# Optimization experiments

Hardware: AMD Instinct MI355X
Metric: run time of the kernel (lower is better)

## Reference

```python
import jax, jax.numpy as jnp
import numpy as np

B, N, C, HEADS, R = 8, 4096, 256, 8, 4  # N = H*W, R = reduction_ratio
LN_EPS = 1e-5


def setup_inputs() -> dict:
    key = jax.random.key(0)
    ks = jax.random.split(key, 6)
    sc = 0.02
    return {
        "x": jax.random.normal(ks[0], (B, N, C), jnp.float32),
        "conv_w": jax.random.normal(ks[1], (C, C, R, R), jnp.float32) * sc,  # OIHW
        "conv_b": jnp.zeros((C,), jnp.float32),
        "ln_g": jnp.ones((C,), jnp.float32),
        "ln_b": jnp.zeros((C,), jnp.float32),
        "kv_w": jax.random.normal(ks[2], (2 * C, C), jnp.float32) * sc,  # torch Linear (out,in)
        "kv_b": jnp.zeros((2 * C,), jnp.float32),
        "q_w": jax.random.normal(ks[3], (C, C), jnp.float32) * sc,
        "q_b": jnp.zeros((C,), jnp.float32),
        "out_w": jax.random.normal(ks[4], (C, C), jnp.float32) * sc,
        "out_b": jnp.zeros((C,), jnp.float32),
        "H": 64,
        "W": 64,
    }


def reference(x, conv_w, conv_b, ln_g, ln_b, kv_w, kv_b, q_w, q_b, out_w, out_b, H, W):
    Bz, Nq, Ch = x.shape
    d = Ch // HEADS
    scale = 1.0 / np.sqrt(float(d)).astype(np.float32)

    # spatial reduction: (B,N,C) -> (B,C,H,W) -> strided conv -> (B, M, C)
    x1 = x.transpose(0, 2, 1).reshape(Bz, Ch, H, W)
    x1 = jax.lax.conv_general_dilated(
        x1, conv_w, window_strides=(R, R), padding="VALID",
        dimension_numbers=("NCHW", "OIHW", "NCHW"))
    x1 = x1 + conv_b[None, :, None, None]
    x1 = x1.reshape(Bz, Ch, -1).transpose(0, 2, 1)  # (B, M, C), M=(H/R)*(W/R)

    # LayerNorm over channels
    mu = x1.mean(-1, keepdims=True)
    var = x1.var(-1, keepdims=True)
    x1 = (x1 - mu) / jnp.sqrt(var + LN_EPS) * ln_g + ln_b

    # K,V from reduced tokens
    kv = x1 @ kv_w.T + kv_b                                  # (B, M, 2C)
    M = kv.shape[1]
    kv = kv.reshape(Bz, M, 2, HEADS, d).transpose(2, 0, 3, 1, 4)  # (2,B,h,M,d)
    k, v = kv[0], kv[1]

    # Q from full-resolution tokens
    q = (x @ q_w.T + q_b).reshape(Bz, Nq, HEADS, d).transpose(0, 2, 1, 3)  # (B,h,N,d)

    attn = jax.nn.softmax(jnp.einsum("bhnd,bhmd->bhnm", q, k) * scale, axis=-1)
    out = jnp.einsum("bhnm,bhmd->bhnd", attn, v)             # (B,h,N,d)
    out = out.transpose(0, 2, 1, 3).reshape(Bz, Nq, Ch)
    return out @ out_w.T + out_b
```

## Files before the change

kernel.cpp:

```cpp
#include <hip/hip_runtime.h>
#include <math.h>

#define LN_EPS 1e-5f
#define SCALE_QK 0.17677669529663687f

using bf16x8 = __bf16 __attribute__((ext_vector_type(8)));
using f32x4 = float __attribute__((ext_vector_type(4)));

__device__ __forceinline__ ushort f2bf(float f) {
  unsigned u = __float_as_uint(f);
  u += 0x7fff + ((u >> 16) & 1);
  return (ushort)(u >> 16);
}

__device__ __forceinline__ unsigned cvt_pk_bf16(float a, float b) {
  unsigned r;
  asm("v_cvt_pk_bf16_f32 %0, %1, %2" : "=v"(r) : "v"(a), "v"(b));
  return r;
}

__device__ __forceinline__ void gload_lds16(const ushort* g, ushort* l) {
  __builtin_amdgcn_global_load_lds((__attribute__((address_space(1))) void*)g,
                                   (__attribute__((address_space(3))) void*)l, 16, 0, 0);
}

__global__ __launch_bounds__(256) void prep_kernel(
    const float* __restrict__ x, ushort* __restrict__ xb,
    const float* __restrict__ qw, const float* __restrict__ kvw,
    const float* __restrict__ ow, const float* __restrict__ cw,
    ushort* __restrict__ qwb, ushort* __restrict__ kvwb,
    ushort* __restrict__ owb, ushort* __restrict__ wTb) {
  int blk = blockIdx.x, tid = threadIdx.x;
  if (blk < 2048) {
    int i = blk * 1024 + tid;
#pragma unroll
    for (int p = 0; p < 4; ++p) {
      float4 v = ((const float4*)x)[i + p * 256];
      ushort4 o = {f2bf(v.x), f2bf(v.y), f2bf(v.z), f2bf(v.w)};
      ((ushort4*)xb)[i + p * 256] = o;
    }
  } else if (blk < 2304) {
    int b2 = blk - 2048;
    const float* src;
    ushort* dst;
    int i;
    if (b2 < 64) { src = qw; dst = qwb; i = b2 * 256 + tid; }
    else if (b2 < 192) { src = kvw; dst = kvwb; i = (b2 - 64) * 256 + tid; }
    else { src = ow; dst = owb; i = (b2 - 192) * 256 + tid; }
    float4 v = ((const float4*)src)[i];
    ushort4 o = {f2bf(v.x), f2bf(v.y), f2bf(v.z), f2bf(v.w)};
    ((ushort4*)dst)[i] = o;
  } else {
    int oc = blk - 2304, ic = tid;
    const float* src = cw + (size_t)oc * 4096 + ic * 16;
#pragma unroll
    for (int pos = 0; pos < 16; ++pos)
      wTb[(size_t)oc * 4096 + pos * 256 + ic] = f2bf(src[pos]);
  }
}

__global__ __launch_bounds__(256, 2) void convq_kernel(
    const ushort* __restrict__ xb, const ushort* __restrict__ wTb,
    float* __restrict__ part, const ushort* __restrict__ qwb,
    const float* __restrict__ qbias, ushort* __restrict__ qbb) {
  __shared__ __attribute__((aligned(16))) ushort As[2][128 * 32];
  __shared__ __attribute__((aligned(16))) ushort Bs[2][64 * 32];
  int tid = threadIdx.x, lane = tid & 63, w = tid >> 6;
  int l15 = lane & 15, quad = lane >> 4;
  int id = blockIdx.x;
  if (id < 256) {
    int m0 = (id & 15) * 128;
    int bz = (id >> 4) & 3;
    int n0 = (id >> 6) * 64;
    int arow0 = w * 16 + (lane >> 2);
    int acol = (lane & 3) * 8;
    f32x4 acc[2][4];
#pragma unroll
    for (int i = 0; i < 2; ++i)
#pragma unroll
      for (int j = 0; j < 4; ++j) acc[i][j] = (f32x4){0.f, 0.f, 0.f, 0.f};

    for (int k0 = 0; k0 < 1024; k0 += 64) {
      int kg = bz * 1024 + k0;
      __syncthreads();
#pragma unroll
      for (int s = 0; s < 2; ++s) {
#pragma unroll
        for (int t = 0; t < 2; ++t) {
          int row = arow0 + t * 64;
          int m = m0 + row;
          int b = m >> 8, mm = m & 255;
          int oh = mm >> 4, ow_ = mm & 15;
          int k = kg + s * 32 + acol;
          int pos = k >> 8, ic = k & 255;
          int n = ((oh << 2) + (pos >> 2)) * 64 + (ow_ << 2) + (pos & 3);
          gload_lds16(xb + ((size_t)(b * 4096 + n) * 256 + ic),
                      &As[s][t * 2048 + w * 512]);
        }
        gload_lds16(wTb + ((size_t)(n0 + w * 16 + (lane >> 2)) * 4096 + kg +
                           s * 32 + acol),
                    &Bs[s][w * 512]);
      }
      __syncthreads();
      int qk = quad * 8;
#pragma unroll
      for (int s = 0; s < 2; ++s) {
        bf16x8 a0 = *(const bf16x8*)&As[s][(w * 32 + l15) * 32 + qk];
        bf16x8 a1 = *(const bf16x8*)&As[s][(w * 32 + 16 + l15) * 32 + qk];
#pragma unroll
        for (int j = 0; j < 4; ++j) {
          bf16x8 bj = *(const bf16x8*)&Bs[s][(j * 16 + l15) * 32 + qk];
          acc[0][j] = __builtin_amdgcn_mfma_f32_16x16x32_bf16(a0, bj, acc[0][j], 0, 0, 0);
          acc[1][j] = __builtin_amdgcn_mfma_f32_16x16x32_bf16(a1, bj, acc[1][j], 0, 0, 0);
        }
      }
    }
    float* Cz = part + (size_t)bz * 524288;
#pragma unroll
    for (int i = 0; i < 2; ++i)
#pragma unroll
      for (int j = 0; j < 4; ++j) {
        int col = n0 + j * 16 + l15;
#pragma unroll
        for (int r = 0; r < 4; ++r) {
          int row = m0 + w * 32 + i * 16 + quad * 4 + r;
          Cz[(size_t)row * 256 + col] = acc[i][j][r];
        }
      }
  } else {
    const float Cc = SCALE_QK * 1.4426950408889634f;
    int qid = id - 256;
    int n0 = (qid >> 7) * 64;
    int m0 = (qid & 127) * 256 + w * 64;
    bf16x8 bfr[4][8];
    const ushort* bbase = qwb + (size_t)(n0 + l15) * 256 + quad * 8;
#pragma unroll
    for (int j = 0; j < 4; ++j)
#pragma unroll
      for (int kc = 0; kc < 8; ++kc)
        bfr[j][kc] = *(const bf16x8*)(bbase + (size_t)j * 16 * 256 + kc * 32);
    float bv[4];
#pragma unroll
    for (int j = 0; j < 4; ++j) bv[j] = qbias[n0 + j * 16 + l15];

#pragma unroll
    for (int t = 0; t < 4; ++t) {
      const ushort* arow = xb + (size_t)(m0 + t * 16 + l15) * 256 + quad * 8;
      bf16x8 af[8];
#pragma unroll
      for (int kc = 0; kc < 8; ++kc) af[kc] = *(const bf16x8*)(arow + kc * 32);
      f32x4 acc[4];
#pragma unroll
      for (int j = 0; j < 4; ++j) acc[j] = (f32x4){0.f, 0.f, 0.f, 0.f};
#pragma unroll
      for (int kc = 0; kc < 8; ++kc)
#pragma unroll
        for (int j = 0; j < 4; ++j)
          acc[j] = __builtin_amdgcn_mfma_f32_16x16x32_bf16(af[kc], bfr[j][kc], acc[j], 0, 0, 0);
#pragma unroll
      for (int j = 0; j < 4; ++j)
#pragma unroll
        for (int r = 0; r < 4; ++r) {
          int row = m0 + t * 16 + quad * 4 + r;
          int col = n0 + j * 16 + l15;
          qbb[(size_t)row * 256 + col] = f2bf((acc[j][r] + bv[j]) * Cc);
        }
    }
  }
}

__global__ __launch_bounds__(256, 2) void breg_gemm_f32(const ushort* __restrict__ A,
                                                        const ushort* __restrict__ Bw,
                                                        const float* __restrict__ bias,
                                                        float* __restrict__ Cf) {
  int tid = threadIdx.x, lane = tid & 63, w = tid >> 6;
  int l15 = lane & 15, quad = lane >> 4;
  int n0 = blockIdx.y * 64;
  int m0 = blockIdx.x * 256 + w * 64;
  bf16x8 bfr[4][8];
  const ushort* bbase = Bw + (size_t)(n0 + l15) * 256 + quad * 8;
#pragma unroll
  for (int j = 0; j < 4; ++j)
#pragma unroll
    for (int kc = 0; kc < 8; ++kc)
      bfr[j][kc] = *(const bf16x8*)(bbase + (size_t)j * 16 * 256 + kc * 32);
  float bv[4];
#pragma unroll
  for (int j = 0; j < 4; ++j) bv[j] = bias[n0 + j * 16 + l15];

#pragma unroll
  for (int t = 0; t < 4; ++t) {
    const ushort* arow = A + (size_t)(m0 + t * 16 + l15) * 256 + quad * 8;
    bf16x8 af[8];
#pragma unroll
    for (int kc = 0; kc < 8; ++kc) af[kc] = *(const bf16x8*)(arow + kc * 32);
    f32x4 acc[4];
#pragma unroll
    for (int j = 0; j < 4; ++j) acc[j] = (f32x4){0.f, 0.f, 0.f, 0.f};
#pragma unroll
    for (int kc = 0; kc < 8; ++kc)
#pragma unroll
      for (int j = 0; j < 4; ++j)
        acc[j] = __builtin_amdgcn_mfma_f32_16x16x32_bf16(af[kc], bfr[j][kc], acc[j], 0, 0, 0);
#pragma unroll
    for (int j = 0; j < 4; ++j)
#pragma unroll
      for (int r = 0; r < 4; ++r) {
        int row = m0 + t * 16 + quad * 4 + r;
        int col = n0 + j * 16 + l15;
        Cf[(size_t)row * 256 + col] = acc[j][r] + bv[j];
      }
  }
}

__global__ __launch_bounds__(256) void ln_fused(const float* __restrict__ part,
                                                const float* __restrict__ cb,
                                                const float* __restrict__ g,
                                                const float* __restrict__ bt,
                                                ushort* __restrict__ x1b) {
  int tid = threadIdx.x;
  int tok = blockIdx.x * 4 + (tid >> 6);
  int lane = tid & 63;
  size_t base = (size_t)tok * 256 + lane * 4;
  float4 c = *(const float4*)(cb + lane * 4);
  float4 v = c;
#pragma unroll
  for (int z = 0; z < 4; ++z) {
    float4 p = *(const float4*)(part + base + (size_t)z * 524288);
    v.x += p.x; v.y += p.y; v.z += p.z; v.w += p.w;
  }
  float s1 = v.x + v.y + v.z + v.w;
  float s2 = v.x * v.x + v.y * v.y + v.z * v.z + v.w * v.w;
#pragma unroll
  for (int o = 1; o < 64; o <<= 1) {
    s1 += __shfl_xor(s1, o, 64);
    s2 += __shfl_xor(s2, o, 64);
  }
  float mu = s1 * (1.f / 256.f);
  float var = s2 * (1.f / 256.f) - mu * mu;
  float rstd = rsqrtf(var + LN_EPS);
  float4 gg = *(const float4*)(g + lane * 4);
  float4 bb = *(const float4*)(bt + lane * 4);
  ushort4 o4 = {f2bf((v.x - mu) * rstd * gg.x + bb.x),
                f2bf((v.y - mu) * rstd * gg.y + bb.y),
                f2bf((v.z - mu) * rstd * gg.z + bb.z),
                f2bf((v.w - mu) * rstd * gg.w + bb.w)};
  *(ushort4*)(x1b + base) = o4;
}

__global__ __launch_bounds__(256) void kv_gemm(const ushort* __restrict__ A,
                                               const ushort* __restrict__ Bw,
                                               const float* __restrict__ bias,
                                               ushort* __restrict__ aux,
                                               ushort* __restrict__ aux2) {
  __shared__ __attribute__((aligned(16))) ushort As[2][128 * 32];
  __shared__ __attribute__((aligned(16))) ushort Bs[2][64 * 32];
  int tid = threadIdx.x;
  int lane = tid & 63, w = tid >> 6;
  int m0 = blockIdx.x * 128, n0 = blockIdx.y * 64;
  int arow0 = w * 16 + (lane >> 2);
  int acol = (lane & 3) * 8;
  f32x4 acc[2][4];
#pragma unroll
  for (int i = 0; i < 2; ++i)
#pragma unroll
    for (int j = 0; j < 4; ++j) acc[i][j] = (f32x4){0.f, 0.f, 0.f, 0.f};

  for (int k0 = 0; k0 < 256; k0 += 64) {
    __syncthreads();
#pragma unroll
    for (int s = 0; s < 2; ++s) {
#pragma unroll
      for (int t = 0; t < 2; ++t) {
        int row = arow0 + t * 64;
        gload_lds16(A + ((size_t)(m0 + row) * 256 + k0 + s * 32 + acol),
                    &As[s][t * 2048 + w * 512]);
      }
      gload_lds16(Bw + ((size_t)(n0 + w * 16 + (lane >> 2)) * 256 + k0 + s * 32 + acol),
                  &Bs[s][w * 512]);
    }
    __syncthreads();
    int qk = (lane >> 4) * 8, l15 = lane & 15;
#pragma unroll
    for (int s = 0; s < 2; ++s) {
      bf16x8 a0 = *(const bf16x8*)&As[s][(w * 32 + l15) * 32 + qk];
      bf16x8 a1 = *(const bf16x8*)&As[s][(w * 32 + 16 + l15) * 32 + qk];
#pragma unroll
      for (int j = 0; j < 4; ++j) {
        bf16x8 bj = *(const bf16x8*)&Bs[s][(j * 16 + l15) * 32 + qk];
        acc[0][j] = __builtin_amdgcn_mfma_f32_16x16x32_bf16(a0, bj, acc[0][j], 0, 0, 0);
        acc[1][j] = __builtin_amdgcn_mfma_f32_16x16x32_bf16(a1, bj, acc[1][j], 0, 0, 0);
      }
    }
  }
  int l15 = lane & 15, q = lane >> 4;
#pragma unroll
  for (int i = 0; i < 2; ++i) {
    int rowb = m0 + w * 32 + i * 16 + q * 4;
    int b = rowb >> 8, mloc = rowb & 255;
#pragma unroll
    for (int j = 0; j < 4; ++j) {
      int col = n0 + j * 16 + l15;
      float bv = bias[col];
      if (col < 256) {
#pragma unroll
        for (int r = 0; r < 4; ++r)
          aux[(size_t)(b * 256 + mloc + r) * 256 + col] = f2bf(acc[i][j][r] + bv);
      } else {
        int c2 = col - 256, h = c2 >> 5, d = c2 & 31;
        unsigned lo = (unsigned)f2bf(acc[i][j][0] + bv) |
                      ((unsigned)f2bf(acc[i][j][1] + bv) << 16);
        unsigned hi = (unsigned)f2bf(acc[i][j][2] + bv) |
                      ((unsigned)f2bf(acc[i][j][3] + bv) << 16);
        *(uint2*)(aux2 + ((size_t)((b * 8 + h) * 32 + d) * 256 + mloc)) =
            make_uint2(lo, hi);
      }
    }
  }
}

__global__ __launch_bounds__(256) void attn_mfma(const ushort* __restrict__ qbb,
                                                 const ushort* __restrict__ kb,
                                                 const ushort* __restrict__ vT,
                                                 ushort* __restrict__ aob) {
  __shared__ __attribute__((aligned(16))) ushort sh[4 * 16 * 264];
  int bid = blockIdx.x;
  int b = bid & 7, h = (bid >> 3) & 7, cp = bid >> 6;
  int tid = threadIdx.x, lane = tid & 63, w = tid >> 6;
  int l15 = lane & 15, quad = lane >> 4;

  {
    const ushort* srcK = kb + (size_t)(b * 256 + w * 64 + (lane >> 2)) * 256 +
                         h * 32 + (lane & 3) * 8;
#pragma unroll
    for (int i = 0; i < 4; ++i)
      gload_lds16(srcK + (size_t)i * 16 * 256, &sh[(w * 64 + i * 16) * 32]);
    const ushort* srcV = vT + (size_t)((b * 8 + h) * 32 + w * 8 + (lane >> 5)) * 256 +
                         (lane & 31) * 8;
#pragma unroll
    for (int i = 0; i < 4; ++i)
      gload_lds16(srcV + (size_t)i * 2 * 256, &sh[8192 + (w * 8 + i * 2) * 256]);
  }
  __syncthreads();
  bf16x8 kf[16];
#pragma unroll
  for (int mt = 0; mt < 16; ++mt)
    kf[mt] = *(const bf16x8*)&sh[(mt * 16 + l15) * 32 + quad * 8];
  bf16x8 vf[2][8];
#pragma unroll
  for (int j = 0; j < 2; ++j)
#pragma unroll
    for (int kc = 0; kc < 8; ++kc)
      vf[j][kc] = *(const bf16x8*)&sh[8192 + (j * 16 + l15) * 256 + kc * 32 + quad * 8];
  __syncthreads();
  ushort* Pw = &sh[w * 16 * 264];

  int q0base = b * 4096 + cp * 512 + w * 64;

  for (int t = 0; t < 8; ++t) {
    int q0 = q0base + ((t & 4) << 6) + (t & 3) * 16;
    bf16x8 qf = *(const bf16x8*)(qbb + (size_t)(q0 + l15) * 256 + h * 32 + quad * 8);
    float lsum = 0.f;
#pragma unroll
    for (int mt = 0; mt < 16; ++mt) {
      f32x4 st = __builtin_amdgcn_mfma_f32_16x16x32_bf16(
          kf[mt], qf, (f32x4){0.f, 0.f, 0.f, 0.f}, 0, 0, 0);
      float e0 = __builtin_amdgcn_exp2f(st[0]);
      float e1 = __builtin_amdgcn_exp2f(st[1]);
      float e2 = __builtin_amdgcn_exp2f(st[2]);
      float e3 = __builtin_amdgcn_exp2f(st[3]);
      lsum += e0 + e1 + e2 + e3;
      unsigned lo = cvt_pk_bf16(e0, e1);
      unsigned hi = cvt_pk_bf16(e2, e3);
      *(uint2*)(Pw + l15 * 264 + mt * 16 + quad * 4) = make_uint2(lo, hi);
    }
    lsum += __shfl_xor(lsum, 16, 64);
    lsum += __shfl_xor(lsum, 32, 64);
    __builtin_amdgcn_s_waitcnt(0xc07f);
    f32x4 oacc[2] = {{0.f, 0.f, 0.f, 0.f}, {0.f, 0.f, 0.f, 0.f}};
#pragma unroll
    for (int kc = 0; kc < 8; ++kc) {
      bf16x8 pf = *(const bf16x8*)(Pw + l15 * 264 + kc * 32 + quad * 8);
      oacc[0] = __builtin_amdgcn_mfma_f32_16x16x32_bf16(pf, vf[0][kc], oacc[0], 0, 0, 0);
      oacc[1] = __builtin_amdgcn_mfma_f32_16x16x32_bf16(pf, vf[1][kc], oacc[1], 0, 0, 0);
    }
    float linv[4];
#pragma unroll
    for (int r = 0; r < 4; ++r)
      linv[r] = __builtin_amdgcn_rcpf(__shfl(lsum, quad * 4 + r, 64));
    ushort* ob = aob + (size_t)q0 * 256 + h * 32;
#pragma unroll
    for (int j = 0; j < 2; ++j)
#pragma unroll
      for (int r = 0; r < 4; ++r) {
        unsigned uo = __float_as_uint(oacc[j][r] * linv[r]) + 0x8000u;
        ob[(size_t)(quad * 4 + r) * 256 + j * 16 + l15] = (ushort)(uo >> 16);
      }
  }
}

extern "C" void kernel_launch(void* const* d_in, const int* in_sizes, int n_in,
                              void* d_out, int out_size, void* d_ws, size_t ws_size,
                              hipStream_t stream) {
  const float* x = (const float*)d_in[0];
  const float* conv_w = (const float*)d_in[1];
  const float* conv_b = (const float*)d_in[2];
  const float* ln_g = (const float*)d_in[3];
  const float* ln_b = (const float*)d_in[4];
  const float* kv_w = (const float*)d_in[5];
  const float* kv_b = (const float*)d_in[6];
  const float* q_w = (const float*)d_in[7];
  const float* q_b = (const float*)d_in[8];
  const float* out_w = (const float*)d_in[9];
  const float* out_b = (const float*)d_in[10];

  ushort* xb = (ushort*)d_ws;
  ushort* wTb = xb + 8388608;
  ushort* qwb = wTb + 1048576;
  ushort* kvwb = qwb + 65536;
  ushort* owb = kvwb + 131072;
  ushort* x1b = owb + 65536;
  ushort* kb = x1b + 524288;
  ushort* vT = kb + 524288;
  ushort* aob = xb;
  float* part = (float*)d_out;
  ushort* qbb = (ushort*)((float*)d_out + 4194304);

  prep_kernel<<<2560, 256, 0, stream>>>(x, xb, q_w, kv_w, out_w, conv_w,
                                        qwb, kvwb, owb, wTb);
  convq_kernel<<<768, 256, 0, stream>>>(xb, wTb, part, qwb, q_b, qbb);
  ln_fused<<<512, 256, 0, stream>>>(part, conv_b, ln_g, ln_b, x1b);
  kv_gemm<<<dim3(16, 8), 256, 0, stream>>>(x1b, kvwb, kv_b, kb, vT);
  attn_mfma<<<512, 256, 0, stream>>>(qbb, kb, vT, aob);
  breg_gemm_f32<<<dim3(128, 4), 256, 0, stream>>>(aob, owb, out_b, (float*)d_out);
}
```

Baseline: 182.9 us.

## Software-pipeline attention tiles with double-buffered P in LDS

Doubles the per-wave P buffer in shared memory so the QK^T and exp stage of the next query tile runs while the PV MFMAs of the current tile proceed. The next Q fragment is prefetched and the loop is fully unrolled, with an explicit lgkmcnt fence and sched barrier before reading P. This aims to hide MFMA and LDS latency across the two stages. The cost is twice the LDS footprint and higher register pressure, which may reduce occupancy.

```diff
diff --git a/kernel.cpp b/kernel.cpp
--- a/kernel.cpp
+++ b/kernel.cpp
@@ -22,6 +22,11 @@
 __device__ __forceinline__ void gload_lds16(const ushort* g, ushort* l) {
   __builtin_amdgcn_global_load_lds((__attribute__((address_space(1))) void*)g,
                                    (__attribute__((address_space(3))) void*)l, 16, 0, 0);
+}
+
+__device__ __forceinline__ void fence_lgkm0() {
+  asm volatile("s_waitcnt lgkmcnt(0)" ::: "memory");
+  __builtin_amdgcn_sched_barrier(0);
 }
 
 __global__ __launch_bounds__(256) void prep_kernel(
@@ -323,7 +328,7 @@
                                                  const ushort* __restrict__ kb,
                                                  const ushort* __restrict__ vT,
                                                  ushort* __restrict__ aob) {
-  __shared__ __attribute__((aligned(16))) ushort sh[4 * 16 * 264];
+  __shared__ __attribute__((aligned(16))) ushort sh[2 * 4 * 16 * 264];
   int bid = blockIdx.x;
   int b = bid & 7, h = (bid >> 3) & 7, cp = bid >> 6;
   int tid = threadIdx.x, lane = tid & 63, w = tid >> 6;
@@ -353,13 +358,12 @@
     for (int kc = 0; kc < 8; ++kc)
       vf[j][kc] = *(const bf16x8*)&sh[8192 + (j * 16 + l15) * 256 + kc * 32 + quad * 8];
   __syncthreads();
-  ushort* Pw = &sh[w * 16 * 264];
+  ushort* Pw0 = &sh[w * 2 * 4224];
+  ushort* Pw1 = Pw0 + 4224;
 
   int q0base = b * 4096 + cp * 512 + w * 64;
 
-  for (int t = 0; t < 8; ++t) {
-    int q0 = q0base + ((t & 4) << 6) + (t & 3) * 16;
-    bf16x8 qf = *(const bf16x8*)(qbb + (size_t)(q0 + l15) * 256 + h * 32 + quad * 8);
+  auto QKEP = [&](bf16x8 qf, ushort* Pw) -> float {
     float lsum = 0.f;
 #pragma unroll
     for (int mt = 0; mt < 16; ++mt) {
@@ -376,18 +380,36 @@
     }
     lsum += __shfl_xor(lsum, 16, 64);
     lsum += __shfl_xor(lsum, 32, 64);
-    __builtin_amdgcn_s_waitcnt(0xc07f);
+    return lsum;
+  };
+  auto qptr = [&](int t) {
+    int q0 = q0base + ((t & 4) << 6) + (t & 3) * 16;
+    return (const bf16x8*)(qbb + (size_t)(q0 + l15) * 256 + h * 32 + quad * 8);
+  };
+
+  float lsum_cur = QKEP(*qptr(0), Pw0);
+
+#pragma unroll
+  for (int t = 0; t < 8; ++t) {
+    ushort* Prd = (t & 1) ? Pw1 : Pw0;
+    ushort* Pwr = (t & 1) ? Pw0 : Pw1;
+    bf16x8 qf_next;
+    if (t < 7) qf_next = *qptr(t + 1);
+    fence_lgkm0();
     f32x4 oacc[2] = {{0.f, 0.f, 0.f, 0.f}, {0.f, 0.f, 0.f, 0.f}};
 #pragma unroll
     for (int kc = 0; kc < 8; ++kc) {
-      bf16x8 pf = *(const bf16x8*)(Pw + l15 * 264 + kc * 32 + quad * 8);
+      bf16x8 pf = *(const bf16x8*)(Prd + l15 * 264 + kc * 32 + quad * 8);
       oacc[0] = __builtin_amdgcn_mfma_f32_16x16x32_bf16(pf, vf[0][kc], oacc[0], 0, 0, 0);
       oacc[1] = __builtin_amdgcn_mfma_f32_16x16x32_bf16(pf, vf[1][kc], oacc[1], 0, 0, 0);
     }
+    float lsum_next = 0.f;
+    if (t < 7) lsum_next = QKEP(qf_next, Pwr);
     float linv[4];
 #pragma unroll
     for (int r = 0; r < 4; ++r)
-      linv[r] = __builtin_amdgcn_rcpf(__shfl(lsum, quad * 4 + r, 64));
+      linv[r] = __builtin_amdgcn_rcpf(__shfl(lsum_cur, quad * 4 + r, 64));
+    int q0 = q0base + ((t & 4) << 6) + (t & 3) * 16;
     ushort* ob = aob + (size_t)q0 * 256 + h * 32;
 #pragma unroll
     for (int j = 0; j < 2; ++j)
@@ -396,6 +418,7 @@
         unsigned uo = __float_as_uint(oacc[j][r] * linv[r]) + 0x8000u;
         ob[(size_t)(quad * 4 + r) * 256 + j * 16 + l15] = (ushort)(uo >> 16);
       }
+    lsum_cur = lsum_next;
   }
 }
 
```

Result: no change. 181.3 us (median of 2 runs) (-0.8%).
